# Performance work log

Hardware: AMD Instinct MI355X
Metric: run time of the kernel (lower is better)

Reference implementation:

```python
import jax, jax.numpy as jnp
import numpy as np

DIM = 256
HEADS = 8
BS = 8
N = 1024
NEG = -1.0e9


def setup_inputs() -> dict:
    key = jax.random.key(0)
    ks = jax.random.split(key, 8)
    feats = jax.random.normal(ks[0], (BS, N, DIM), dtype=jnp.float32)
    adj_mat = (jax.random.uniform(ks[1], (BS, N, N)) < 0.1).astype(jnp.float32)
    s = 1.0 / np.sqrt(DIM)
    fc_w = jax.random.normal(ks[2], (DIM, DIM * HEADS), dtype=jnp.float32) * s
    fc_b = jnp.zeros((DIM * HEADS,), dtype=jnp.float32)
    q_w = jax.random.normal(ks[3], (DIM, 1), dtype=jnp.float32) * s
    q_b = jnp.zeros((1,), dtype=jnp.float32)
    k_w = jax.random.normal(ks[4], (DIM, 1), dtype=jnp.float32) * s
    k_b = jnp.zeros((1,), dtype=jnp.float32)
    fp_w = jax.random.normal(ks[5], (DIM * HEADS, DIM), dtype=jnp.float32) * (1.0 / np.sqrt(DIM * HEADS))
    fp_b = jnp.zeros((DIM,), dtype=jnp.float32)
    return {"feats": feats, "adj_mat": adj_mat, "fc_w": fc_w, "fc_b": fc_b,
            "q_w": q_w, "q_b": q_b, "k_w": k_w, "k_b": k_b,
            "fp_w": fp_w, "fp_b": fp_b}


def reference(feats, adj_mat, fc_w, fc_b, q_w, q_b, k_w, k_b, fp_w, fp_b):
    bs, n, dim = feats.shape
    # [bs, N, heads*dim] -> [bs, heads, N, dim]
    feat_proj = (feats @ fc_w + fc_b).reshape(bs, n, HEADS, dim).transpose(0, 2, 1, 3)
    q = feat_proj @ q_w + q_b            # [bs, heads, N, 1]
    k = feat_proj @ k_w + k_b            # [bs, heads, N, 1]
    logits = q + jnp.swapaxes(k, -1, -2)  # additive scores [bs, heads, N, N]
    masked = logits + (1.0 - adj_mat[:, None]) * NEG
    masked = jax.nn.leaky_relu(masked, negative_slope=0.01)
    attn = jax.nn.softmax(masked, axis=-1)  # dropout is identity at eval
    out = attn @ feat_proj                   # [bs, heads, N, dim]
    out = out.transpose(0, 2, 1, 3).reshape(bs, n, HEADS * dim)
    out = out @ fp_w + fp_b + feats          # residual=True
    return jax.nn.sigmoid(out)
```

## Files before the change

kernel.cpp:

```cpp
#include <hip/hip_runtime.h>
#include <hip/hip_bf16.h>

typedef unsigned short u16;
typedef unsigned int u32;
typedef unsigned long long u64;
typedef __attribute__((ext_vector_type(8))) short short8;
typedef __attribute__((ext_vector_type(4))) float floatx4;
typedef const __attribute__((address_space(1))) void* gp_t;
typedef __attribute__((address_space(3))) void* sp_t;

static __device__ __forceinline__ u16 f2bf(float x) {
    __hip_bfloat16 h = __float2bfloat16(x);
    union { __hip_bfloat16 h; u16 u; } cv; cv.h = h; return cv.u;
}

__global__ __launch_bounds__(256)
void k_prepall(const float* __restrict__ feats, const float* __restrict__ adj,
               const float* __restrict__ fc_w, const float* __restrict__ fc_b,
               const float* __restrict__ q_w, const float* __restrict__ q_b,
               const float* __restrict__ k_w, const float* __restrict__ k_b,
               const float* __restrict__ fp_w,
               u16* __restrict__ feats2, u16* __restrict__ maskH,
               u16* __restrict__ fcw2, u16* __restrict__ fpw2,
               u16* __restrict__ W, float* __restrict__ C) {
    __shared__ float shbuf[64 * 65];
    int id = blockIdx.x, t = threadIdx.x;
    if (id < 2048) {
        long g = (long)id * 256 + t;
        const float4* ap = (const float4*)adj + g * 4;
        u32 mm = 0;
        #pragma unroll
        for (int w = 0; w < 4; w++) {
            float4 f = ap[w];
            mm |= (f.x > 0.f ? 1u : 0u) << (4 * w);
            mm |= (f.y > 0.f ? 1u : 0u) << (4 * w + 1);
            mm |= (f.z > 0.f ? 1u : 0u) << (4 * w + 2);
            mm |= (f.w > 0.f ? 1u : 0u) << (4 * w + 3);
        }
        maskH[g] = (u16)mm;
    } else if (id < 3072) {
        int n = (id - 2048) * 8 + (t >> 5), c = t & 31;
        const float* src = feats + (long)n * 256 + c * 8;
        float4 f0 = *(const float4*)src, f1 = *(const float4*)(src + 4);
        u16 tmp[8] = {f2bf(f0.x), f2bf(f0.y), f2bf(f0.z), f2bf(f0.w),
                      f2bf(f1.x), f2bf(f1.y), f2bf(f1.z), f2bf(f1.w)};
        *(int4*)&feats2[(long)c * 65536 + n * 8] = *(int4*)tmp;
    } else if (id < 3200) {
        int b = id - 3072, bx = b & 31, by = b >> 5;
        float (*tt)[65] = (float(*)[65])shbuf;
        int c = t & 63, r0 = t >> 6;
        for (int rr = r0; rr < 64; rr += 4)
            tt[rr][c] = fc_w[(long)(by * 64 + rr) * 2048 + bx * 64 + c];
        __syncthreads();
        int hdl = t & 63;
        #pragma unroll
        for (int oo = 0; oo < 2; oo++) {
            int o = (t >> 6) + oo * 4;
            u16 tmp[8];
            #pragma unroll
            for (int e = 0; e < 8; e++) tmp[e] = f2bf(tt[o * 8 + e][hdl]);
            *(int4*)&fcw2[(long)(by * 8 + o) * 16384 + (bx * 64 + hdl) * 8] = *(int4*)tmp;
        }
    } else if (id < 3328) {
        int b = id - 3200, bx = b & 3, by = b >> 2;
        float (*tt)[65] = (float(*)[65])shbuf;
        int c = t & 63, r0 = t >> 6;
        for (int rr = r0; rr < 64; rr += 4)
            tt[rr][c] = fp_w[(long)(by * 64 + rr) * 256 + bx * 64 + c];
        __syncthreads();
        int cl = t & 63;
        #pragma unroll
        for (int oo = 0; oo < 2; oo++) {
            int o = (t >> 6) + oo * 4;
            u16 tmp[8];
            #pragma unroll
            for (int e = 0; e < 8; e++) tmp[e] = f2bf(tt[o * 8 + e][cl]);
            *(int4*)&fpw2[(long)(by * 8 + o) * 2048 + (bx * 64 + cl) * 8] = *(int4*)tmp;
        }
    } else {
        int t2 = id - 3328, x = t2 & 15, dq = t2 >> 4;
        int h = x & 7, kind = x >> 3;
        const float* w = kind ? k_w : q_w;
        float* ws_ = shbuf;
        ws_[t] = w[t];
        __syncthreads();
        int dl = t >> 2, part = t & 3;
        int d = dq * 64 + dl;
        const float* row = fc_w + (long)d * 2048 + h * 256 + part * 64;
        float a = 0.f;
        #pragma unroll 8
        for (int i = 0; i < 64; i++) a += row[i] * ws_[part * 64 + i];
        a += __shfl_xor(a, 1);
        a += __shfl_xor(a, 2);
        if (part == 0) W[(long)x * 256 + d] = f2bf(a);
        if (t == 0 && dq == 0) {
            float cb = 0.f;
            const float* fb = fc_b + h * 256;
            for (int i = 0; i < 256; i++) cb += fb[i] * ws_[i];
            C[x] = cb + (kind ? k_b[0] : q_b[0]);
        }
    }
}

__global__ __launch_bounds__(256)
void k_g1qk(const u16* __restrict__ fcw2, const u16* __restrict__ feats2,
            const float* __restrict__ bias, u16* __restrict__ V2,
            const u16* __restrict__ Wb, const float* __restrict__ C,
            float* __restrict__ qo, float* __restrict__ ko) {
    int tid = threadIdx.x, wave = tid >> 6, lane = tid & 63;
    int q = lane >> 4, n16 = lane & 15;

    if (blockIdx.y >= 16) {
        int blk = (blockIdx.y - 16) * 64 + blockIdx.x;
        int rowBase = blk * 64 + wave * 16;
        floatx4 acc = {};
        #pragma unroll
        for (int k0 = 0; k0 < 256; k0 += 32) {
            short8 af = *(const short8*)&feats2[(long)((k0 >> 3) + q) * 65536
                                                + (rowBase + n16) * 8];
            short8 bf = *(const short8*)&Wb[n16 * 256 + k0 + q * 8];
            acc = __builtin_amdgcn_mfma_f32_16x16x32_bf16(af, bf, acc, 0, 0, 0);
        }
        float cc = C[n16];
        #pragma unroll
        for (int r = 0; r < 4; r++) {
            int gr = rowBase + q * 4 + r;
            int b = gr >> 10, nn = gr & 1023;
            float v = acc[r] + cc;
            if (n16 < 8) qo[((b * 8 + n16) << 10) + nn] = v;
            else         ko[((b * 8 + (n16 - 8)) << 10) + nn] = v;
        }
        return;
    }

    __shared__ u16 As[2][4 * 128 * 8];
    __shared__ u16 Bs[2][4 * 128 * 8];
    int rowBase = blockIdx.y * 128;
    int colBase = blockIdx.x * 128;
    int wr = wave >> 1, wc = wave & 1;
    floatx4 acc[4][4] = {};

    auto dma = [&](int k0, int p) {
        int kc = k0 >> 3;
        #pragma unroll
        for (int r = 0; r < 2; r++) {
            __builtin_amdgcn_global_load_lds(
                (gp_t)&fcw2[(long)(kc + wave) * 16384 + (rowBase + r * 64 + lane) * 8],
                (sp_t)&As[p][(wave * 128 + r * 64 + lane) * 8], 16, 0, 0);
            __builtin_amdgcn_global_load_lds(
                (gp_t)&feats2[(long)(kc + wave) * 65536 + (colBase + r * 64 + lane) * 8],
                (sp_t)&Bs[p][(wave * 128 + r * 64 + lane) * 8], 16, 0, 0);
        }
    };

    dma(0, 0);
    __syncthreads();
    for (int k0 = 0; k0 < 256; k0 += 32) {
        int p = (k0 >> 5) & 1;
        short8 af[4], bfr[4];
        #pragma unroll
        for (int i = 0; i < 4; i++)
            af[i] = *(short8*)&As[p][(q * 128 + wr * 64 + i * 16 + n16) * 8];
        #pragma unroll
        for (int i = 0; i < 4; i++)
            bfr[i] = *(short8*)&Bs[p][(q * 128 + wc * 64 + i * 16 + n16) * 8];
        if (k0 + 32 < 256) dma(k0 + 32, p ^ 1);
        #pragma unroll
        for (int mi = 0; mi < 4; mi++)
            #pragma unroll
            for (int ni = 0; ni < 4; ni++)
                acc[mi][ni] = __builtin_amdgcn_mfma_f32_16x16x32_bf16(
                    af[mi], bfr[ni], acc[mi][ni], 0, 0, 0);
        __syncthreads();
    }

    #pragma unroll
    for (int mi = 0; mi < 4; mi++) {
        #pragma unroll
        for (int r = 0; r < 4; r++) {
            int grow = rowBase + wr * 64 + mi * 16 + q * 4 + r;
            int h = grow >> 8, d = grow & 255;
            float bv = bias[grow];
            #pragma unroll
            for (int ni = 0; ni < 4; ni++) {
                int gcol = colBase + wc * 64 + ni * 16 + n16;
                int b = gcol >> 10, nn = gcol & 1023;
                V2[(((long)(b * 8 + h)) << 18) + (nn >> 3) * 2048 + d * 8 + (nn & 7)]
                    = f2bf(acc[mi][ni][r] + bv);
            }
        }
    }
}

__global__ __launch_bounds__(512)
__attribute__((amdgpu_waves_per_eu(4)))
void k_attn(const u32* __restrict__ maskW, const float* __restrict__ qv,
            const float* __restrict__ kv, const u16* __restrict__ fpjT2,
            u16* __restrict__ outh2) {
    __shared__ u16 As[2][128 * 40];
    __shared__ u16 Bs[2][4 * 256 * 8];
    __shared__ float qS[128], kS[1024], lsumS[512], rlS[128];

    int z = blockIdx.x;
    int b = z >> 3, h = z & 7;
    int i0 = blockIdx.y * 128;
    int tid = threadIdx.x;
    int wave = tid >> 6, lane = tid & 63;
    int wr = wave >> 2, wc = wave & 3;
    int q  = lane >> 4, n16 = lane & 15;

    if (tid < 256) *(float4*)&kS[tid * 4] = *(const float4*)&kv[(z << 10) + tid * 4];
    if (tid >= 256 && tid < 384) qS[tid - 256] = qv[(z << 10) + i0 + (tid - 256)];

    floatx4 acc[4][4] = {};
    int ar = tid >> 2;
    int jq = (tid & 3) * 8;
    const u32* mrow = maskW + (((long)(b << 10) + i0 + ar) << 5);
    const u16* Vbase = fpjT2 + ((long)z << 18);
    float lsum = 0.f;

    auto dma_v = [&](int k0, int p) {
        #pragma unroll
        for (int t = 0; t < 2; t++) {
            int s = wave * 2 + t;
            __builtin_amdgcn_global_load_lds(
                (gp_t)&Vbase[((k0 >> 3) + (s >> 2)) * 2048 + ((s & 3) * 64 + lane) * 8],
                (sp_t)&Bs[p][((s >> 2) * 256 + (s & 3) * 64 + lane) * 8],
                16, 0, 0);
        }
    };

    __syncthreads();
    float qi = qS[ar];

    auto stage_p = [&](int p, u32 mw, float4 kA, float4 kB) {
        float kk[8] = {kA.x, kA.y, kA.z, kA.w, kB.x, kB.y, kB.z, kB.w};
        u32 pw[4];
        #pragma unroll
        for (int e2 = 0; e2 < 4; e2++) {
            float s0 = qi + kk[2 * e2];
            s0 = fmaxf(s0, 0.01f * s0);
            float p0 = ((mw >> (2 * e2)) & 1u) ? __expf(s0) : 0.f;
            float s1 = qi + kk[2 * e2 + 1];
            s1 = fmaxf(s1, 0.01f * s1);
            float p1 = ((mw >> (2 * e2 + 1)) & 1u) ? __expf(s1) : 0.f;
            lsum += p0 + p1;
            pw[e2] = __builtin_amdgcn_perm(__float_as_uint(p1), __float_as_uint(p0),
                                           0x07060302);
        }
        *(int4*)&As[p][ar * 40 + jq] = *(int4*)&pw[0];
    };

    {
        u32 mw0 = mrow[0] >> jq;
        float4 kA0 = *(const float4*)&kS[jq];
        float4 kB0 = *(const float4*)&kS[jq + 4];
        dma_v(0, 0);
        stage_p(0, mw0, kA0, kB0);
    }
    __syncthreads();

    for (int k0 = 0; k0 < 1024; k0 += 32) {
        int p = (k0 >> 5) & 1;
        int kn = (k0 + 32 < 1024) ? k0 + 32 : 0;
        u32 mw = mrow[kn >> 5] >> jq;
        float4 kA = *(const float4*)&kS[kn + jq];
        float4 kB = *(const float4*)&kS[kn + jq + 4];
        short8 af[4], bfr[4];
        #pragma unroll
        for (int i = 0; i < 4; i++)
            af[i] = *(short8*)&As[p][(wr * 64 + i * 16 + n16) * 40 + q * 8];
        #pragma unroll
        for (int i = 0; i < 4; i++)
            bfr[i] = *(short8*)&Bs[p][(q * 256 + wc * 64 + i * 16 + n16) * 8];
        if (k0 + 32 < 1024) {
            dma_v(k0 + 32, p ^ 1);
            stage_p(p ^ 1, mw, kA, kB);
        }
        #pragma unroll
        for (int mi = 0; mi < 4; mi++)
            #pragma unroll
            for (int ni = 0; ni < 4; ni++)
                acc[mi][ni] = __builtin_amdgcn_mfma_f32_16x16x32_bf16(
                    af[mi], bfr[ni], acc[mi][ni], 0, 0, 0);
        __syncthreads();
    }

    lsumS[tid] = lsum;
    __syncthreads();
    if (tid < 128) {
        float l = lsumS[4 * tid] + lsumS[4 * tid + 1] +
                  lsumS[4 * tid + 2] + lsumS[4 * tid + 3];
        rlS[tid] = l > 0.f ? 1.f / l : 0.f;
    }
    __syncthreads();

    #pragma unroll
    for (int mi = 0; mi < 4; mi++) {
        #pragma unroll
        for (int r = 0; r < 4; r++) {
            int grow = wr * 64 + mi * 16 + q * 4 + r;
            float s = rlS[grow];
            long row = (long)(b * 1024 + i0 + grow);
            #pragma unroll
            for (int ni = 0; ni < 4; ni++) {
                int gcol = wc * 64 + ni * 16 + n16;
                outh2[((long)(h * 32 + (gcol >> 3)) << 16) + row * 8 + (gcol & 7)]
                    = f2bf(acc[mi][ni][r] * s);
            }
        }
    }
}

__global__ __launch_bounds__(256)
void k_g3(const u16* __restrict__ A2,
          const u16* __restrict__ B2,
          const float* __restrict__ bias,
          const float* __restrict__ resid,
          float* __restrict__ out) {
    __shared__ u16 As[2][8 * 64 * 8];
    __shared__ u16 Bs[2][8 * 64 * 8];
    int rowBase = blockIdx.x * 64;
    int colBase = blockIdx.y * 64;
    int tid = threadIdx.x, wave = tid >> 6, lane = tid & 63;
    int wr = wave >> 1, wc = wave & 1;
    int q = lane >> 4, n16 = lane & 15;
    floatx4 acc[2][2] = {};

    auto dma = [&](int k0, int p) {
        int kc = k0 >> 3;
        #pragma unroll
        for (int s = 0; s < 2; s++) {
            int c = wave + s * 4;
            __builtin_amdgcn_global_load_lds(
                (gp_t)&A2[(long)(kc + c) * 65536 + (rowBase + lane) * 8],
                (sp_t)&As[p][(c * 64 + lane) * 8], 16, 0, 0);
            __builtin_amdgcn_global_load_lds(
                (gp_t)&B2[(long)(kc + c) * 2048 + (colBase + lane) * 8],
                (sp_t)&Bs[p][(c * 64 + lane) * 8], 16, 0, 0);
        }
    };

    dma(0, 0);
    __syncthreads();
    for (int k0 = 0; k0 < 2048; k0 += 64) {
        int p = (k0 >> 6) & 1;
        short8 af[2][2], bfr[2][2];
        #pragma unroll
        for (int kf = 0; kf < 2; kf++)
            #pragma unroll
            for (int i = 0; i < 2; i++) {
                af[kf][i]  = *(short8*)&As[p][((kf * 4 + q) * 64 + wr * 32 + i * 16 + n16) * 8];
                bfr[kf][i] = *(short8*)&Bs[p][((kf * 4 + q) * 64 + wc * 32 + i * 16 + n16) * 8];
            }
        if (k0 + 64 < 2048) dma(k0 + 64, p ^ 1);
        #pragma unroll
        for (int kf = 0; kf < 2; kf++)
            #pragma unroll
            for (int mi = 0; mi < 2; mi++)
                #pragma unroll
                for (int ni = 0; ni < 2; ni++)
                    acc[mi][ni] = __builtin_amdgcn_mfma_f32_16x16x32_bf16(
                        af[kf][mi], bfr[kf][ni], acc[mi][ni], 0, 0, 0);
        __syncthreads();
    }

    #pragma unroll
    for (int mi = 0; mi < 2; mi++) {
        #pragma unroll
        for (int r = 0; r < 4; r++) {
            int grow = rowBase + wr * 32 + mi * 16 + q * 4 + r;
            #pragma unroll
            for (int ni = 0; ni < 2; ni++) {
                int gcol = colBase + wc * 32 + ni * 16 + n16;
                float v = acc[mi][ni][r] + bias[gcol] + resid[(long)grow * 256 + gcol];
                out[(long)grow * 256 + gcol] = 1.f / (1.f + __expf(-v));
            }
        }
    }
}

extern "C" void kernel_launch(void* const* d_in, const int* in_sizes, int n_in,
                              void* d_out, int out_size, void* d_ws, size_t ws_size,
                              hipStream_t stream) {
    const float* feats = (const float*)d_in[0];
    const float* adj   = (const float*)d_in[1];
    const float* fc_w  = (const float*)d_in[2];
    const float* fc_b  = (const float*)d_in[3];
    const float* q_w   = (const float*)d_in[4];
    const float* q_b   = (const float*)d_in[5];
    const float* k_w   = (const float*)d_in[6];
    const float* k_b   = (const float*)d_in[7];
    const float* fp_w  = (const float*)d_in[8];
    const float* fp_b  = (const float*)d_in[9];

    char* ws = (char*)d_ws;
    u16*   feats2 = (u16*)ws;   ws += (size_t)2097152 * 2;
    u16*   fcw2   = (u16*)ws;   ws += (size_t)524288 * 2;
    u16*   fpw2   = (u16*)ws;   ws += (size_t)524288 * 2;
    u16*   fpjT2  = (u16*)ws;   ws += (size_t)16777216 * 2;
    float* qv     = (float*)ws; ws += (size_t)65536 * 4;
    float* kv     = (float*)ws; ws += (size_t)65536 * 4;
    u16*   outh2  = (u16*)ws;   ws += (size_t)16777216 * 2;
    u64*   maskB  = (u64*)ws;   ws += (size_t)131072 * 8;
    u16*   Weff   = (u16*)ws;   ws += (size_t)4096 * 2;
    float* Ceff   = (float*)ws; ws += (size_t)16 * 4;

    k_prepall<<<3392, 256, 0, stream>>>(feats, adj, fc_w, fc_b, q_w, q_b,
                                        k_w, k_b, fp_w,
                                        feats2, (u16*)maskB, fcw2, fpw2, Weff, Ceff);

    k_g1qk<<<dim3(64, 18), 256, 0, stream>>>(fcw2, feats2, fc_b, fpjT2,
                                             Weff, Ceff, qv, kv);

    k_attn<<<dim3(64, 8), 512, 0, stream>>>((const u32*)maskB, qv, kv, fpjT2, outh2);

    k_g3<<<dim3(128, 4), 256, 0, stream>>>(outh2, fpw2, fp_b, feats, (float*)d_out);
}
```

Before: 195.0 us.

## Stage GEMM epilogues through LDS, use raw exp2, retile output GEMM

The q/k logits are pre-scaled by log2(e) so the attention softmax can use the raw v_exp_f32 instruction instead of __expf. The epilogues of the projection GEMM and the attention kernel now write bf16 tiles into shared memory first and then store them as coalesced 16-byte chunks, replacing scattered 2-byte global writes. The final projection GEMM uses 64x32 tiles with one wave per 16 rows, which doubles the grid to increase parallelism. This trades extra LDS traffic and barriers for better global store efficiency. Because leaky_relu is positively homogeneous, scaling before it preserves the result.

```diff
diff --git a/kernel.cpp b/kernel.cpp
--- a/kernel.cpp
+++ b/kernel.cpp
@@ -8,6 +8,12 @@
 typedef __attribute__((ext_vector_type(4))) float floatx4;
 typedef const __attribute__((address_space(1))) void* gp_t;
 typedef __attribute__((address_space(3))) void* sp_t;
+
+#define LOG2E 1.44269504088896f
+
+static __device__ __forceinline__ float exp2_raw(float x) {
+    float r; asm("v_exp_f32 %0, %1" : "=v"(r) : "v"(x)); return r;
+}
 
 static __device__ __forceinline__ u16 f2bf(float x) {
     __hip_bfloat16 h = __float2bfloat16(x);
@@ -107,6 +113,7 @@
             const float* __restrict__ bias, u16* __restrict__ V2,
             const u16* __restrict__ Wb, const float* __restrict__ C,
             float* __restrict__ qo, float* __restrict__ ko) {
+    __shared__ u16 smem[16896];
     int tid = threadIdx.x, wave = tid >> 6, lane = tid & 63;
     int q = lane >> 4, n16 = lane & 15;
 
@@ -126,15 +133,13 @@
         for (int r = 0; r < 4; r++) {
             int gr = rowBase + q * 4 + r;
             int b = gr >> 10, nn = gr & 1023;
-            float v = acc[r] + cc;
+            float v = (acc[r] + cc) * LOG2E;
             if (n16 < 8) qo[((b * 8 + n16) << 10) + nn] = v;
             else         ko[((b * 8 + (n16 - 8)) << 10) + nn] = v;
         }
         return;
     }
 
-    __shared__ u16 As[2][4 * 128 * 8];
-    __shared__ u16 Bs[2][4 * 128 * 8];
     int rowBase = blockIdx.y * 128;
     int colBase = blockIdx.x * 128;
     int wr = wave >> 1, wc = wave & 1;
@@ -142,14 +147,16 @@
 
     auto dma = [&](int k0, int p) {
         int kc = k0 >> 3;
+        u16* Ab = smem + p * 4096;
+        u16* Bb = smem + 8192 + p * 4096;
         #pragma unroll
         for (int r = 0; r < 2; r++) {
             __builtin_amdgcn_global_load_lds(
                 (gp_t)&fcw2[(long)(kc + wave) * 16384 + (rowBase + r * 64 + lane) * 8],
-                (sp_t)&As[p][(wave * 128 + r * 64 + lane) * 8], 16, 0, 0);
+                (sp_t)&Ab[(wave * 128 + r * 64 + lane) * 8], 16, 0, 0);
             __builtin_amdgcn_global_load_lds(
                 (gp_t)&feats2[(long)(kc + wave) * 65536 + (colBase + r * 64 + lane) * 8],
-                (sp_t)&Bs[p][(wave * 128 + r * 64 + lane) * 8], 16, 0, 0);
+                (sp_t)&Bb[(wave * 128 + r * 64 + lane) * 8], 16, 0, 0);
         }
     };
 
@@ -157,13 +164,15 @@
     __syncthreads();
     for (int k0 = 0; k0 < 256; k0 += 32) {
         int p = (k0 >> 5) & 1;
+        u16* Ab = smem + p * 4096;
+        u16* Bb = smem + 8192 + p * 4096;
         short8 af[4], bfr[4];
         #pragma unroll
         for (int i = 0; i < 4; i++)
-            af[i] = *(short8*)&As[p][(q * 128 + wr * 64 + i * 16 + n16) * 8];
+            af[i] = *(short8*)&Ab[(q * 128 + wr * 64 + i * 16 + n16) * 8];
         #pragma unroll
         for (int i = 0; i < 4; i++)
-            bfr[i] = *(short8*)&Bs[p][(q * 128 + wc * 64 + i * 16 + n16) * 8];
+            bfr[i] = *(short8*)&Bb[(q * 128 + wc * 64 + i * 16 + n16) * 8];
         if (k0 + 32 < 256) dma(k0 + 32, p ^ 1);
         #pragma unroll
         for (int mi = 0; mi < 4; mi++)
@@ -174,21 +183,30 @@
         __syncthreads();
     }
 
+    u16* eb = smem;
     #pragma unroll
     for (int mi = 0; mi < 4; mi++) {
         #pragma unroll
         for (int r = 0; r < 4; r++) {
-            int grow = rowBase + wr * 64 + mi * 16 + q * 4 + r;
-            int h = grow >> 8, d = grow & 255;
-            float bv = bias[grow];
+            int d_loc = wr * 64 + mi * 16 + q * 4 + r;
+            float bv = bias[rowBase + d_loc];
             #pragma unroll
             for (int ni = 0; ni < 4; ni++) {
-                int gcol = colBase + wc * 64 + ni * 16 + n16;
-                int b = gcol >> 10, nn = gcol & 1023;
-                V2[(((long)(b * 8 + h)) << 18) + (nn >> 3) * 2048 + d * 8 + (nn & 7)]
-                    = f2bf(acc[mi][ni][r] + bv);
+                int nn_loc = wc * 64 + ni * 16 + n16;
+                eb[d_loc * 132 + nn_loc] = f2bf(acc[mi][ni][r] + bv);
             }
         }
+    }
+    __syncthreads();
+    int hB = rowBase >> 8, dB = rowBase & 255;
+    int bB = colBase >> 10, cB = (colBase & 1023) >> 3;
+    long vbase = ((long)(bB * 8 + hB)) << 18;
+    #pragma unroll
+    for (int j = 0; j < 8; j++) {
+        int idx = j * 256 + tid;
+        int dl = idx & 127, c8 = idx >> 7;
+        *(int4*)&V2[vbase + (long)(cB + c8) * 2048 + (dB + dl) * 8]
+            = *(int4*)&eb[dl * 132 + c8 * 8];
     }
 }
 
@@ -197,8 +215,7 @@
 void k_attn(const u32* __restrict__ maskW, const float* __restrict__ qv,
             const float* __restrict__ kv, const u16* __restrict__ fpjT2,
             u16* __restrict__ outh2) {
-    __shared__ u16 As[2][128 * 40];
-    __shared__ u16 Bs[2][4 * 256 * 8];
+    __shared__ u16 smem[26624];
     __shared__ float qS[128], kS[1024], lsumS[512], rlS[128];
 
     int z = blockIdx.x;
@@ -220,12 +237,13 @@
     float lsum = 0.f;
 
     auto dma_v = [&](int k0, int p) {
+        u16* Bb = smem + 10240 + p * 8192;
         #pragma unroll
         for (int t = 0; t < 2; t++) {
             int s = wave * 2 + t;
             __builtin_amdgcn_global_load_lds(
                 (gp_t)&Vbase[((k0 >> 3) + (s >> 2)) * 2048 + ((s & 3) * 64 + lane) * 8],
-                (sp_t)&Bs[p][((s >> 2) * 256 + (s & 3) * 64 + lane) * 8],
+                (sp_t)&Bb[((s >> 2) * 256 + (s & 3) * 64 + lane) * 8],
                 16, 0, 0);
         }
     };
@@ -234,21 +252,22 @@
     float qi = qS[ar];
 
     auto stage_p = [&](int p, u32 mw, float4 kA, float4 kB) {
+        u16* Ab = smem + p * 5120;
         float kk[8] = {kA.x, kA.y, kA.z, kA.w, kB.x, kB.y, kB.z, kB.w};
         u32 pw[4];
         #pragma unroll
         for (int e2 = 0; e2 < 4; e2++) {
             float s0 = qi + kk[2 * e2];
             s0 = fmaxf(s0, 0.01f * s0);
-            float p0 = ((mw >> (2 * e2)) & 1u) ? __expf(s0) : 0.f;
+            float p0 = ((mw >> (2 * e2)) & 1u) ? exp2_raw(s0) : 0.f;
             float s1 = qi + kk[2 * e2 + 1];
             s1 = fmaxf(s1, 0.01f * s1);
-            float p1 = ((mw >> (2 * e2 + 1)) & 1u) ? __expf(s1) : 0.f;
+            float p1 = ((mw >> (2 * e2 + 1)) & 1u) ? exp2_raw(s1) : 0.f;
             lsum += p0 + p1;
             pw[e2] = __builtin_amdgcn_perm(__float_as_uint(p1), __float_as_uint(p0),
                                            0x07060302);
         }
-        *(int4*)&As[p][ar * 40 + jq] = *(int4*)&pw[0];
+        *(int4*)&Ab[ar * 40 + jq] = *(int4*)&pw[0];
     };
 
     {
@@ -262,6 +281,8 @@
 
     for (int k0 = 0; k0 < 1024; k0 += 32) {
         int p = (k0 >> 5) & 1;
+        u16* Ab = smem + p * 5120;
+        u16* Bb = smem + 10240 + p * 8192;
         int kn = (k0 + 32 < 1024) ? k0 + 32 : 0;
         u32 mw = mrow[kn >> 5] >> jq;
         float4 kA = *(const float4*)&kS[kn + jq];
@@ -269,10 +290,10 @@
         short8 af[4], bfr[4];
         #pragma unroll
         for (int i = 0; i < 4; i++)
-            af[i] = *(short8*)&As[p][(wr * 64 + i * 16 + n16) * 40 + q * 8];
+            af[i] = *(short8*)&Ab[(wr * 64 + i * 16 + n16) * 40 + q * 8];
         #pragma unroll
         for (int i = 0; i < 4; i++)
-            bfr[i] = *(short8*)&Bs[p][(q * 256 + wc * 64 + i * 16 + n16) * 8];
+            bfr[i] = *(short8*)&Bb[(q * 256 + wc * 64 + i * 16 + n16) * 8];
         if (k0 + 32 < 1024) {
             dma_v(k0 + 32, p ^ 1);
             stage_p(p ^ 1, mw, kA, kB);
@@ -295,20 +316,35 @@
     }
     __syncthreads();
 
+    u16* eb = smem;
+    long rowG = (long)(b * 1024 + i0);
     #pragma unroll
-    for (int mi = 0; mi < 4; mi++) {
-        #pragma unroll
-        for (int r = 0; r < 4; r++) {
-            int grow = wr * 64 + mi * 16 + q * 4 + r;
-            float s = rlS[grow];
-            long row = (long)(b * 1024 + i0 + grow);
-            #pragma unroll
-            for (int ni = 0; ni < 4; ni++) {
-                int gcol = wc * 64 + ni * 16 + n16;
-                outh2[((long)(h * 32 + (gcol >> 3)) << 16) + row * 8 + (gcol & 7)]
-                    = f2bf(acc[mi][ni][r] * s);
+    for (int hh = 0; hh < 2; hh++) {
+        if ((wc >> 1) == hh) {
+            #pragma unroll
+            for (int mi = 0; mi < 4; mi++) {
+                #pragma unroll
+                for (int r = 0; r < 4; r++) {
+                    int grow = wr * 64 + mi * 16 + q * 4 + r;
+                    float s = rlS[grow];
+                    #pragma unroll
+                    for (int ni = 0; ni < 4; ni++) {
+                        int col = (wc & 1) * 64 + ni * 16 + n16;
+                        eb[grow * 132 + col] = f2bf(acc[mi][ni][r] * s);
+                    }
+                }
             }
         }
+        __syncthreads();
+        #pragma unroll
+        for (int j = 0; j < 4; j++) {
+            int idx = j * 512 + tid;
+            int row = idx & 127, c8 = idx >> 7;
+            int chunk = h * 32 + hh * 16 + c8;
+            *(int4*)&outh2[((long)chunk << 16) + (rowG + row) * 8]
+                = *(int4*)&eb[row * 132 + c8 * 8];
+        }
+        __syncthreads();
     }
 }
 
@@ -319,63 +355,58 @@
           const float* __restrict__ resid,
           float* __restrict__ out) {
     __shared__ u16 As[2][8 * 64 * 8];
-    __shared__ u16 Bs[2][8 * 64 * 8];
+    __shared__ u16 Bs[2][8 * 32 * 8];
     int rowBase = blockIdx.x * 64;
-    int colBase = blockIdx.y * 64;
+    int colBase = blockIdx.y * 32;
     int tid = threadIdx.x, wave = tid >> 6, lane = tid & 63;
-    int wr = wave >> 1, wc = wave & 1;
     int q = lane >> 4, n16 = lane & 15;
-    floatx4 acc[2][2] = {};
+    floatx4 acc[2] = {};
 
     auto dma = [&](int k0, int p) {
         int kc = k0 >> 3;
         #pragma unroll
-        for (int s = 0; s < 2; s++) {
-            int c = wave + s * 4;
+        for (int t = 0; t < 2; t++) {
+            int c = wave + t * 4;
             __builtin_amdgcn_global_load_lds(
                 (gp_t)&A2[(long)(kc + c) * 65536 + (rowBase + lane) * 8],
                 (sp_t)&As[p][(c * 64 + lane) * 8], 16, 0, 0);
-            __builtin_amdgcn_global_load_lds(
-                (gp_t)&B2[(long)(kc + c) * 2048 + (colBase + lane) * 8],
-                (sp_t)&Bs[p][(c * 64 + lane) * 8], 16, 0, 0);
-        }
+        }
+        __builtin_amdgcn_global_load_lds(
+            (gp_t)&B2[(long)(kc + wave * 2 + (lane >> 5)) * 2048
+                      + (colBase + (lane & 31)) * 8],
+            (sp_t)&Bs[p][(wave * 64 + lane) * 8], 16, 0, 0);
     };
 
     dma(0, 0);
     __syncthreads();
     for (int k0 = 0; k0 < 2048; k0 += 64) {
         int p = (k0 >> 6) & 1;
-        short8 af[2][2], bfr[2][2];
+        short8 af[2], bfr[2][2];
+        #pragma unroll
+        for (int kf = 0; kf < 2; kf++) {
+            af[kf] = *(short8*)&As[p][((kf * 4 + q) * 64 + wave * 16 + n16) * 8];
+            #pragma unroll
+            for (int nf = 0; nf < 2; nf++)
+                bfr[kf][nf] = *(short8*)&Bs[p][((kf * 4 + q) * 32 + nf * 16 + n16) * 8];
+        }
+        if (k0 + 64 < 2048) dma(k0 + 64, p ^ 1);
         #pragma unroll
         for (int kf = 0; kf < 2; kf++)
             #pragma unroll
-            for (int i = 0; i < 2; i++) {
-                af[kf][i]  = *(short8*)&As[p][((kf * 4 + q) * 64 + wr * 32 + i * 16 + n16) * 8];
-                bfr[kf][i] = *(short8*)&Bs[p][((kf * 4 + q) * 64 + wc * 32 + i * 16 + n16) * 8];
-            }
-        if (k0 + 64 < 2048) dma(k0 + 64, p ^ 1);
-        #pragma unroll
-        for (int kf = 0; kf < 2; kf++)
-            #pragma unroll
-            for (int mi = 0; mi < 2; mi++)
-                #pragma unroll
-                for (int ni = 0; ni < 2; ni++)
-                    acc[mi][ni] = __builtin_amdgcn_mfma_f32_16x16x32_bf16(
-                        af[kf][mi], bfr[kf][ni], acc[mi][ni], 0, 0, 0);
+            for (int nf = 0; nf < 2; nf++)
+                acc[nf] = __builtin_amdgcn_mfma_f32_16x16x32_bf16(
+                    af[kf], bfr[kf][nf], acc[nf], 0, 0, 0);
         __syncthreads();
     }
 
     #pragma unroll
-    for (int mi = 0; mi < 2; mi++) {
+    for (int nf = 0; nf < 2; nf++) {
         #pragma unroll
         for (int r = 0; r < 4; r++) {
-            int grow = rowBase + wr * 32 + mi * 16 + q * 4 + r;
-            #pragma unroll
-            for (int ni = 0; ni < 2; ni++) {
-                int gcol = colBase + wc * 32 + ni * 16 + n16;
-                float v = acc[mi][ni][r] + bias[gcol] + resid[(long)grow * 256 + gcol];
-                out[(long)grow * 256 + gcol] = 1.f / (1.f + __expf(-v));
-            }
+            int grow = rowBase + wave * 16 + q * 4 + r;
+            int gcol = colBase + nf * 16 + n16;
+            float v = acc[nf][r] + bias[gcol] + resid[(long)grow * 256 + gcol];
+            out[(long)grow * 256 + gcol] = 1.f / (1.f + __expf(-v));
         }
     }
 }
@@ -415,5 +446,5 @@
 
     k_attn<<<dim3(64, 8), 512, 0, stream>>>((const u32*)maskB, qv, kv, fpjT2, outh2);
 
-    k_g3<<<dim3(128, 4), 256, 0, stream>>>(outh2, fpw2, fp_b, feats, (float*)d_out);
-}
+    k_g3<<<dim3(128, 8), 256, 0, stream>>>(outh2, fpw2, fp_b, feats, (float*)d_out);
+}
```

Measured after the change: 186.3 us. 1.05x faster.
